# Performance work log

Hardware: AMD Instinct MI355X
Metric: run time of the kernel (lower is better)

Reference implementation:

```python
import jax, jax.numpy as jnp
import numpy as np

B, N, S, C, H = 16, 64, 4096, 768, 8
HD = C // H
SCALE = HD ** -0.5
ASSIGN_EPS = 1.0


def hard_softmax(logits, axis):
    # softmax over `axis`, then straight-through one-hot argmax along `axis`
    y_soft = jax.nn.softmax(logits, axis=axis)
    idx = jnp.argmax(y_soft, axis=axis, keepdims=True)
    n = logits.shape[axis]
    shape = [1] * logits.ndim
    shape[axis] = n
    iota = jnp.arange(n).reshape(shape)
    y_hard = (iota == idx).astype(logits.dtype)
    return y_hard - jax.lax.stop_gradient(y_soft) + y_soft


def setup_inputs() -> dict:
    key = jax.random.key(0)
    ks = jax.random.split(key, 7)
    w = lambda k, shp: (jax.random.normal(k, shp, dtype=jnp.float32) * 0.02)
    return {
        'query': jax.random.normal(ks[0], (B, N, C), dtype=jnp.float32),
        'key_in': jax.random.normal(ks[1], (B, S, C), dtype=jnp.float32),
        'Wq': w(ks[2], (C, C)),
        'Wk': w(ks[3], (C, C)),
        'Wv': w(ks[4], (C, C)),
        'Wo': w(ks[5], (C, C)),
        'bo': jnp.zeros((C,), dtype=jnp.float32),
    }


def reference(query, key_in, Wq, Wk, Wv, Wo, bo):
    # linear projections (torch Linear: x @ W.T), split heads -> b h n d
    q = jnp.einsum('bnc,dc->bnd', query, Wq).reshape(B, N, H, HD).transpose(0, 2, 1, 3)
    k = jnp.einsum('bsc,dc->bsd', key_in, Wk).reshape(B, S, H, HD).transpose(0, 2, 1, 3)
    v = jnp.einsum('bsc,dc->bsd', key_in, Wv).reshape(B, S, H, HD).transpose(0, 2, 1, 3)
    raw_attn = jnp.einsum('bhnd,bhsd->bhns', q, k) * SCALE      # [B,H,N,S]
    attn = hard_softmax(raw_attn, axis=-2)                       # hard assign over groups N
    attn = attn / (attn.sum(axis=-1, keepdims=True) + ASSIGN_EPS)  # renorm over tokens S
    out = jnp.einsum('bhns,bhsd->bhnd', attn, v)                 # [B,H,N,HD]
    out = out.transpose(0, 2, 1, 3).reshape(B, N, C)
    out = jnp.einsum('bnc,dc->bnd', out, Wo) + bo
    return out
```

## Files before the change

kernel.cpp:

```cpp
#include <hip/hip_runtime.h>

#define BB 16
#define NN 64
#define SS 4096
#define CC 768
#define HH 8
#define HD 96

typedef __attribute__((ext_vector_type(8))) short bf16x8;
typedef __attribute__((ext_vector_type(4))) float f32x4;
typedef __attribute__((ext_vector_type(8))) unsigned short u16x8;

static __device__ __forceinline__ unsigned short f2bf(float x) {
  unsigned u = __float_as_uint(x);
  unsigned r = (u + 0x7fffu + ((u >> 16) & 1u)) >> 16;
  return (unsigned short)r;
}
static __device__ __forceinline__ float bf2f(unsigned short h) {
  return __uint_as_float(((unsigned)h) << 16);
}
static __device__ __forceinline__ void split2t(float f0, float f1,
                                               unsigned* hw, unsigned* lw) {
  unsigned u0 = __float_as_uint(f0), u1 = __float_as_uint(f1);
  *hw = (u0 >> 16) | (u1 & 0xffff0000u);
  float l0 = f0 - __uint_as_float(u0 & 0xffff0000u);
  float l1 = f1 - __uint_as_float(u1 & 0xffff0000u);
  unsigned v0 = __float_as_uint(l0), v1 = __float_as_uint(l1);
  *lw = (v0 >> 16) | (v1 & 0xffff0000u);
}

__global__ __launch_bounds__(256) void k_transpose(
    const float* __restrict__ src, float* __restrict__ dst) {
  __shared__ float tile[32][33];
  const int bx = blockIdx.x % 24, by = blockIdx.x / 24;
  const int tx = threadIdx.x & 31, ty = threadIdx.x >> 5;
#pragma unroll
  for (int k = 0; k < 4; ++k)
    tile[ty + k * 8][tx] = src[(size_t)(by * 32 + ty + k * 8) * CC + bx * 32 + tx];
  __syncthreads();
#pragma unroll
  for (int k = 0; k < 4; ++k)
    dst[(size_t)(bx * 32 + ty + k * 8) * CC + by * 32 + tx] = tile[tx][ty + k * 8];
}

__global__ __launch_bounds__(256) void k_q(
    const float* __restrict__ query, const float* __restrict__ WqT,
    double* __restrict__ q64g) {
  __shared__ double qin[2][CC];
  const int tid = threadIdx.x;
  const int rp = blockIdx.x / 3, cs = blockIdx.x % 3;
  const int r0 = rp * 2;

#pragma unroll
  for (int u = 0; u < 6; ++u) {
    int idx = tid + u * 256;
    int r = idx / CC, c = idx - r * CC;
    qin[r][c] = (double)query[(size_t)(r0 + r) * CC + c];
  }
  __syncthreads();

  const int j = cs * 256 + tid;
  double a0 = 0.0, a1 = 0.0;
  const float* wt = WqT + j;
  for (int e = 0; e < CC; ++e) {
    const double w = (double)wt[(size_t)e * CC];
    a0 += qin[0][e] * w;
    a1 += qin[1][e] * w;
  }
  q64g[(size_t)(r0 + 0) * CC + j] = a0;
  q64g[(size_t)(r0 + 1) * CC + j] = a1;
}

__global__ __launch_bounds__(256) void k_fold(
    const double* __restrict__ q64g, const float* __restrict__ Wk,
    double* __restrict__ qk64, unsigned short* __restrict__ qhp,
    unsigned short* __restrict__ qlp) {
  __shared__ double q64l[2][CC];
  const int tid = threadIdx.x;
  const int rp = blockIdx.x / 3, cs3 = blockIdx.x % 3;
  const int r0 = rp * 2;

#pragma unroll
  for (int u = 0; u < 6; ++u) {
    int idx = tid + u * 256;
    int r = idx / CC, c = idx - r * CC;
    q64l[r][c] = q64g[(size_t)(r0 + r) * CC + c];
  }
  __syncthreads();

  const int c = cs3 * 256 + tid;
  const double SC = 0.10206207261596575;
  const int csp = c >> 5, lkc = (c >> 3) & 3, jp = c & 7;

  for (int h = 0; h < HH; ++h) {
    double b0 = 0.0, b1 = 0.0;
    const float* wk = Wk + (size_t)(h * HD) * CC + c;
    const double* qh0 = &q64l[0][h * HD];
    const double* qh1 = &q64l[1][h * HD];
#pragma unroll 4
    for (int dd = 0; dd < HD; ++dd) {
      const double w = (double)wk[(size_t)dd * CC];
      b0 += qh0[dd] * w;
      b1 += qh1[dd] * w;
    }
    b0 *= SC; b1 *= SC;
    double av[2] = {b0, b1};
#pragma unroll
    for (int r = 0; r < 2; ++r) {
      const int row = r0 + r, b_ = row >> 6, n = row & 63;
      const int col512 = h * 64 + n;
      size_t o = ((size_t)(b_ * HH + h) * NN + n) * CC + c;
      qk64[o] = av[r];
      float f = (float)av[r];
      unsigned short hh16 = f2bf(f);
      size_t po = (((size_t)(b_ * 24 + csp) * 32 + (col512 >> 4)) * 64 +
                   (lkc * 16 + (col512 & 15))) * 8 + jp;
      qhp[po] = hh16;
      qlp[po] = f2bf(f - bf2f(hh16));
    }
  }
}

#define DELTA 1e-3f

__global__ __launch_bounds__(512) void k_filter_mfma(
    const float* __restrict__ key,
    const unsigned short* __restrict__ qhp, const unsigned short* __restrict__ qlp,
    unsigned char* __restrict__ assign_t, int* __restrict__ susp,
    int* __restrict__ scnt) {
  __shared__ unsigned short khi[2][64][72];
  __shared__ unsigned short klo[2][64][72];
  const int tid = threadIdx.x;
  const int lane = tid & 63;
  const int wn = tid >> 6;
  const int bid0 = blockIdx.x;
  const int swz = (bid0 & 7) * 128 + (bid0 >> 3);
  const int b = swz >> 6;
  const int s0 = (swz & 63) * 64;
  const int l16 = lane & 15;
  const int lk = lane >> 4;

  f32x4 acc[4][4];
#pragma unroll
  for (int m = 0; m < 4; ++m)
#pragma unroll
    for (int n = 0; n < 4; ++n) acc[m][n] = (f32x4){0.f, 0.f, 0.f, 0.f};

  const float* kbase = key + ((size_t)b * SS + s0) * CC;
  const int srow = tid >> 3, sc8 = tid & 7;

#define BBASE(cs) ((((size_t)(b * 24 + (cs)) * 32 + wn * 4) * 64 + lane) * 8)

  bf16x8 bhA[4], blA[4], bhB[4], blB[4];
  {
    float4 st0 = *(const float4*)(kbase + (size_t)srow * CC + sc8 * 8);
    float4 st1 = *(const float4*)(kbase + (size_t)srow * CC + sc8 * 8 + 4);
    union { u16x8 v; unsigned w[4]; } h8, l8;
    split2t(st0.x, st0.y, &h8.w[0], &l8.w[0]);
    split2t(st0.z, st0.w, &h8.w[1], &l8.w[1]);
    split2t(st1.x, st1.y, &h8.w[2], &l8.w[2]);
    split2t(st1.z, st1.w, &h8.w[3], &l8.w[3]);
    *(u16x8*)&khi[0][srow][sc8 * 8] = h8.v;
    *(u16x8*)&klo[0][srow][sc8 * 8] = l8.v;
    const size_t bb = BBASE(0);
#pragma unroll
    for (int n = 0; n < 4; ++n) {
      bhA[n] = *(const bf16x8*)(qhp + bb + (size_t)n * 512);
      blA[n] = *(const bf16x8*)(qlp + bb + (size_t)n * 512);
    }
  }
  __syncthreads();

  for (int t = 0; t < 12; ++t) {
    const int cur = t & 1;
    float4 st0, st1;
    if (t < 11) {
      const int cb = (t + 1) * 64;
      st0 = *(const float4*)(kbase + (size_t)srow * CC + cb + sc8 * 8);
      st1 = *(const float4*)(kbase + (size_t)srow * CC + cb + sc8 * 8 + 4);
    }
    {
      const int cs = t * 2;
      const size_t bbn = BBASE(cs + 1);
#pragma unroll
      for (int n = 0; n < 4; ++n) {
        bhB[n] = *(const bf16x8*)(qhp + bbn + (size_t)n * 512);
        blB[n] = *(const bf16x8*)(qlp + bbn + (size_t)n * 512);
      }
      bf16x8 ah[4], al_[4];
#pragma unroll
      for (int m = 0; m < 4; ++m) {
        ah[m]  = *(const bf16x8*)&khi[cur][m * 16 + l16][lk * 8];
        al_[m] = *(const bf16x8*)&klo[cur][m * 16 + l16][lk * 8];
      }
#pragma unroll
      for (int m = 0; m < 4; ++m)
#pragma unroll
        for (int n = 0; n < 4; ++n)
          acc[m][n] = __builtin_amdgcn_mfma_f32_16x16x32_bf16(ah[m], bhA[n], acc[m][n], 0, 0, 0);
#pragma unroll
      for (int m = 0; m < 4; ++m)
#pragma unroll
        for (int n = 0; n < 4; ++n)
          acc[m][n] = __builtin_amdgcn_mfma_f32_16x16x32_bf16(ah[m], blA[n], acc[m][n], 0, 0, 0);
#pragma unroll
      for (int m = 0; m < 4; ++m)
#pragma unroll
        for (int n = 0; n < 4; ++n)
          acc[m][n] = __builtin_amdgcn_mfma_f32_16x16x32_bf16(al_[m], bhA[n], acc[m][n], 0, 0, 0);
    }
    {
      if (t < 11) {
        const size_t bbn = BBASE(t * 2 + 2);
#pragma unroll
        for (int n = 0; n < 4; ++n) {
          bhA[n] = *(const bf16x8*)(qhp + bbn + (size_t)n * 512);
          blA[n] = *(const bf16x8*)(qlp + bbn + (size_t)n * 512);
        }
      }
      bf16x8 ah[4], al_[4];
#pragma unroll
      for (int m = 0; m < 4; ++m) {
        ah[m]  = *(const bf16x8*)&khi[cur][m * 16 + l16][32 + lk * 8];
        al_[m] = *(const bf16x8*)&klo[cur][m * 16 + l16][32 + lk * 8];
      }
#pragma unroll
      for (int m = 0; m < 4; ++m)
#pragma unroll
        for (int n = 0; n < 4; ++n)
          acc[m][n] = __builtin_amdgcn_mfma_f32_16x16x32_bf16(ah[m], bhB[n], acc[m][n], 0, 0, 0);
#pragma unroll
      for (int m = 0; m < 4; ++m)
#pragma unroll
        for (int n = 0; n < 4; ++n)
          acc[m][n] = __builtin_amdgcn_mfma_f32_16x16x32_bf16(ah[m], blB[n], acc[m][n], 0, 0, 0);
#pragma unroll
      for (int m = 0; m < 4; ++m)
#pragma unroll
        for (int n = 0; n < 4; ++n)
          acc[m][n] = __builtin_amdgcn_mfma_f32_16x16x32_bf16(al_[m], bhB[n], acc[m][n], 0, 0, 0);
    }

    if (t < 11) {
      union { u16x8 v; unsigned w[4]; } h8, l8;
      split2t(st0.x, st0.y, &h8.w[0], &l8.w[0]);
      split2t(st0.z, st0.w, &h8.w[1], &l8.w[1]);
      split2t(st1.x, st1.y, &h8.w[2], &l8.w[2]);
      split2t(st1.z, st1.w, &h8.w[3], &l8.w[3]);
      *(u16x8*)&khi[cur ^ 1][srow][sc8 * 8] = h8.v;
      *(u16x8*)&klo[cur ^ 1][srow][sc8 * 8] = l8.v;
    }
    __syncthreads();
  }
#undef BBASE

#pragma unroll
  for (int m = 0; m < 4; ++m) {
    const int tokbase = s0 + m * 16 + lk * 4;
#pragma unroll
    for (int r = 0; r < 4; ++r) {
      const int tok = tokbase + r;
      float m1 = -3.402823466e38f, m2 = -3.402823466e38f;
      int i1 = 0;
#pragma unroll
      for (int n = 0; n < 4; ++n) {
        float v = acc[m][n][r];
        int g = n * 16 + l16;
        if (v > m1) { m2 = m1; m1 = v; i1 = g; }
        else if (v > m2) m2 = v;
      }
#pragma unroll
      for (int off = 1; off <= 8; off <<= 1) {
        float om1 = __shfl_xor(m1, off);
        float om2 = __shfl_xor(m2, off);
        int oi1 = __shfl_xor(i1, off);
        if (om1 > m1 || (om1 == m1 && oi1 < i1)) {
          m2 = fmaxf(m1, fmaxf(m2, om2));
          m1 = om1; i1 = oi1;
        } else {
          m2 = fmaxf(om1, fmaxf(m2, om2));
        }
      }
      if (l16 == 0) {
        const int bh2 = b * 8 + wn;
        assign_t[((size_t)b * SS + tok) * 8 + wn] = (unsigned char)i1;
        if (m1 - m2 < DELTA) {
          int w = atomicAdd(&scnt[bh2], 1);
          susp[(size_t)bh2 * SS + w] = tok;
        }
      }
    }
  }
}

__global__ __launch_bounds__(256) void k_rescore(
    const float* __restrict__ key, const double* __restrict__ qk64,
    const int* __restrict__ susp, const int* __restrict__ scnt,
    unsigned char* __restrict__ assign_t) {
  __shared__ float krow[16][CC];
  __shared__ double l64[16][64];
  const int bh = blockIdx.x;
  const int cnt = scnt[bh];
  if (cnt == 0) return;
  const int b = bh >> 3, h = bh & 7;
  const int tid = threadIdx.x;
  const int n = tid >> 2, q = tid & 3;
  const double* qrow = qk64 + ((size_t)bh * NN + n) * CC + q * 192;

  for (int i0 = 0; i0 < cnt; i0 += 16) {
    const int nb = (cnt - i0 < 16) ? (cnt - i0) : 16;
    for (int r = 0; r < nb; ++r) {
      const int s = susp[(size_t)bh * SS + i0 + r];
      for (int u = tid; u < CC; u += 256)
        krow[r][u] = key[((size_t)b * SS + s) * CC + u];
    }
    __syncthreads();

    double acc[16];
#pragma unroll
    for (int r = 0; r < 16; ++r) acc[r] = 0.0;
    for (int c4 = 0; c4 < 48; ++c4) {
      const double w0 = qrow[c4 * 4 + 0];
      const double w1 = qrow[c4 * 4 + 1];
      const double w2 = qrow[c4 * 4 + 2];
      const double w3 = qrow[c4 * 4 + 3];
#pragma unroll
      for (int r = 0; r < 16; ++r) {
        float4 k4 = *(const float4*)&krow[r][q * 192 + c4 * 4];
        acc[r] += w0 * (double)k4.x;
        acc[r] += w1 * (double)k4.y;
        acc[r] += w2 * (double)k4.z;
        acc[r] += w3 * (double)k4.w;
      }
    }
#pragma unroll
    for (int r = 0; r < 16; ++r) {
      acc[r] += __shfl_xor(acc[r], 1);
      acc[r] += __shfl_xor(acc[r], 2);
    }
    if (q == 0) {
#pragma unroll
      for (int r = 0; r < 16; ++r) l64[r][n] = acc[r];
    }
    __syncthreads();
    if (tid < nb) {
      double best = l64[tid][0];
      int bi = 0;
      for (int n2 = 1; n2 < 64; ++n2)
        if (l64[tid][n2] > best) { best = l64[tid][n2]; bi = n2; }
      const int s = susp[(size_t)bh * SS + i0 + tid];
      assign_t[((size_t)b * SS + s) * 8 + h] = (unsigned char)bi;
    }
    __syncthreads();
  }
}

__global__ __launch_bounds__(256) void k_counts(
    const unsigned char* __restrict__ assign_t, int* __restrict__ counts) {
  __shared__ int hist[64];
  const int bh = blockIdx.x;
  const int b = bh >> 3, h = bh & 7;
  const int tid = threadIdx.x;
  if (tid < 64) hist[tid] = 0;
  __syncthreads();
  for (int s = tid; s < SS; s += 256)
    atomicAdd(&hist[assign_t[((size_t)b * SS + s) * 8 + h]], 1);
  __syncthreads();
  if (tid < 64) counts[bh * 64 + tid] = hist[tid];
}

__global__ __launch_bounds__(256) void k_convert(
    const float* __restrict__ keyhalf, unsigned short* __restrict__ kb16) {
  const int n8 = 8 * SS * CC / 8;
  int i = blockIdx.x * 256 + threadIdx.x;
  const int stride = gridDim.x * 256;
  for (; i < n8; i += stride) {
    float4 a = ((const float4*)keyhalf)[i * 2];
    float4 b = ((const float4*)keyhalf)[i * 2 + 1];
    u16x8 r;
    r[0] = f2bf(a.x); r[1] = f2bf(a.y); r[2] = f2bf(a.z); r[3] = f2bf(a.w);
    r[4] = f2bf(b.x); r[5] = f2bf(b.y); r[6] = f2bf(b.z); r[7] = f2bf(b.w);
    *(u16x8*)(kb16 + (size_t)i * 8) = r;
  }
}

__global__ __launch_bounds__(64) void k_rank(
    const unsigned char* __restrict__ assign_t, const int* __restrict__ counts,
    int* __restrict__ offsets, int* __restrict__ perm) {
  __shared__ int base[64];
  const int bh = blockIdx.x;
  const int b = bh >> 3, h = bh & 7;
  const int lane = threadIdx.x;

  int cn = counts[bh * 64 + lane];
  int off = cn;
#pragma unroll
  for (int d = 1; d < 64; d <<= 1) {
    int t = __shfl_up(off, d);
    if (lane >= d) off += t;
  }
  off -= cn;
  offsets[bh * 64 + lane] = off;
  base[lane] = off;

  for (int c = 0; c < SS / 64; ++c) {
    const int s = c * 64 + lane;
    const int g = (int)assign_t[((size_t)b * SS + s) * 8 + h];
    unsigned long long m = ~0ull;
#pragma unroll
    for (int k = 0; k < 6; ++k) {
      unsigned long long bk = __ballot((g >> k) & 1);
      m &= ((g >> k) & 1) ? bk : ~bk;
    }
    const int leader = __ffsll((unsigned long long)m) - 1;
    const int rankin = __popcll(m & ((1ull << lane) - 1ull));
    int baseo = 0;
    if (lane == leader) {
      baseo = base[g];
      base[g] = baseo + __popcll(m);
    }
    baseo = __shfl(baseo, leader);
    perm[(size_t)bh * SS + baseo + rankin] = s;
  }
}

__global__ __launch_bounds__(64) void k_gatherp(
    const unsigned short* __restrict__ kb16, const int* __restrict__ perm,
    const int* __restrict__ offsets, const int* __restrict__ counts,
    float* __restrict__ gsum, int b0) {
  const int bid = blockIdx.x;
  const int bl = bid >> 9;
  const int gbid = b0 * 512 + bid;
  const int bh = gbid >> 6;
  const int lane = threadIdx.x;

  const int off = offsets[gbid];
  const int cnt = counts[gbid];
  const int* pl = perm + (size_t)bh * SS + off;
  const unsigned short* kb = kb16 + (size_t)bl * SS * CC;

  float4 a0 = {0.f, 0.f, 0.f, 0.f}, b0v = a0, c0 = a0;
  int j = 0;
  for (; j + 3 < cnt; j += 4) {
    const int s0 = pl[j], s1 = pl[j + 1], s2 = pl[j + 2], s3 = pl[j + 3];
    const ushort4* k0 = (const ushort4*)(kb + (size_t)s0 * CC);
    const ushort4* k1 = (const ushort4*)(kb + (size_t)s1 * CC);
    const ushort4* k2 = (const ushort4*)(kb + (size_t)s2 * CC);
    const ushort4* k3 = (const ushort4*)(kb + (size_t)s3 * CC);
    ushort4 x0 = k0[lane], x1 = k0[lane + 64], x2 = k0[lane + 128];
    ushort4 y0 = k1[lane], y1 = k1[lane + 64], y2 = k1[lane + 128];
    ushort4 z0 = k2[lane], z1 = k2[lane + 64], z2 = k2[lane + 128];
    ushort4 w0 = k3[lane], w1 = k3[lane + 64], w2 = k3[lane + 128];
    a0.x += bf2f(x0.x); a0.y += bf2f(x0.y); a0.z += bf2f(x0.z); a0.w += bf2f(x0.w);
    b0v.x += bf2f(x1.x); b0v.y += bf2f(x1.y); b0v.z += bf2f(x1.z); b0v.w += bf2f(x1.w);
    c0.x += bf2f(x2.x); c0.y += bf2f(x2.y); c0.z += bf2f(x2.z); c0.w += bf2f(x2.w);
    a0.x += bf2f(y0.x); a0.y += bf2f(y0.y); a0.z += bf2f(y0.z); a0.w += bf2f(y0.w);
    b0v.x += bf2f(y1.x); b0v.y += bf2f(y1.y); b0v.z += bf2f(y1.z); b0v.w += bf2f(y1.w);
    c0.x += bf2f(y2.x); c0.y += bf2f(y2.y); c0.z += bf2f(y2.z); c0.w += bf2f(y2.w);
    a0.x += bf2f(z0.x); a0.y += bf2f(z0.y); a0.z += bf2f(z0.z); a0.w += bf2f(z0.w);
    b0v.x += bf2f(z1.x); b0v.y += bf2f(z1.y); b0v.z += bf2f(z1.z); b0v.w += bf2f(z1.w);
    c0.x += bf2f(z2.x); c0.y += bf2f(z2.y); c0.z += bf2f(z2.z); c0.w += bf2f(z2.w);
    a0.x += bf2f(w0.x); a0.y += bf2f(w0.y); a0.z += bf2f(w0.z); a0.w += bf2f(w0.w);
    b0v.x += bf2f(w1.x); b0v.y += bf2f(w1.y); b0v.z += bf2f(w1.z); b0v.w += bf2f(w1.w);
    c0.x += bf2f(w2.x); c0.y += bf2f(w2.y); c0.z += bf2f(w2.z); c0.w += bf2f(w2.w);
  }
  for (; j < cnt; ++j) {
    const int s0 = pl[j];
    const ushort4* k0 = (const ushort4*)(kb + (size_t)s0 * CC);
    ushort4 x0 = k0[lane], x1 = k0[lane + 64], x2 = k0[lane + 128];
    a0.x += bf2f(x0.x); a0.y += bf2f(x0.y); a0.z += bf2f(x0.z); a0.w += bf2f(x0.w);
    b0v.x += bf2f(x1.x); b0v.y += bf2f(x1.y); b0v.z += bf2f(x1.z); b0v.w += bf2f(x1.w);
    c0.x += bf2f(x2.x); c0.y += bf2f(x2.y); c0.z += bf2f(x2.z); c0.w += bf2f(x2.w);
  }
  float4* go = (float4*)(gsum + (size_t)gbid * CC);
  go[lane] = a0; go[lane + 64] = b0v; go[lane + 128] = c0;
}

__global__ __launch_bounds__(256) void k_out(
    const float* __restrict__ gsum, const int* __restrict__ counts,
    const float* __restrict__ WvT, const float* __restrict__ WoT,
    const float* __restrict__ bo, float* __restrict__ out) {
  __shared__ float gs[2][HH][CC];
  __shared__ float vr[2][CC];
  const int tid = threadIdx.x;
  const int r0 = blockIdx.x * 2;

  for (int r = 0; r < 2; ++r) {
    int row = r0 + r, b = row >> 6, n = row & 63;
    for (int h = 0; h < HH; ++h) {
      const float sc = 1.f / (float)(counts[(b * HH + h) * NN + n] + 1);
      const float* src = gsum + ((size_t)(b * HH + h) * NN + n) * CC;
      for (int m = 0; m < 3; ++m)
        gs[r][h][tid + m * 256] = src[tid + m * 256] * sc;
    }
  }
  __syncthreads();

  const int h0 = tid / HD, h1 = (tid + 256) / HD, h2 = (tid + 512) / HD;
  {
    float a00 = 0.f, a01 = 0.f, a02 = 0.f;
    float a10 = 0.f, a11 = 0.f, a12 = 0.f;
    const float* wt = WvT + tid;
    for (int e4 = 0; e4 < CC / 4; ++e4) {
      const int e = e4 * 4;
      float4 g00 = *(const float4*)&gs[0][h0][e];
      float4 g01 = *(const float4*)&gs[0][h1][e];
      float4 g02 = *(const float4*)&gs[0][h2][e];
      float4 g10 = *(const float4*)&gs[1][h0][e];
      float4 g11 = *(const float4*)&gs[1][h1][e];
      float4 g12 = *(const float4*)&gs[1][h2][e];
      const float* w0p = wt + (size_t)e * CC;
      const float* w1p = wt + (size_t)(e + 1) * CC;
      const float* w2p = wt + (size_t)(e + 2) * CC;
      const float* w3p = wt + (size_t)(e + 3) * CC;
      float wa = w0p[0], wb = w0p[256], wc = w0p[512];
      a00 = fmaf(g00.x, wa, a00); a01 = fmaf(g01.x, wb, a01); a02 = fmaf(g02.x, wc, a02);
      a10 = fmaf(g10.x, wa, a10); a11 = fmaf(g11.x, wb, a11); a12 = fmaf(g12.x, wc, a12);
      wa = w1p[0]; wb = w1p[256]; wc = w1p[512];
      a00 = fmaf(g00.y, wa, a00); a01 = fmaf(g01.y, wb, a01); a02 = fmaf(g02.y, wc, a02);
      a10 = fmaf(g10.y, wa, a10); a11 = fmaf(g11.y, wb, a11); a12 = fmaf(g12.y, wc, a12);
      wa = w2p[0]; wb = w2p[256]; wc = w2p[512];
      a00 = fmaf(g00.z, wa, a00); a01 = fmaf(g01.z, wb, a01); a02 = fmaf(g02.z, wc, a02);
      a10 = fmaf(g10.z, wa, a10); a11 = fmaf(g11.z, wb, a11); a12 = fmaf(g12.z, wc, a12);
      wa = w3p[0]; wb = w3p[256]; wc = w3p[512];
      a00 = fmaf(g00.w, wa, a00); a01 = fmaf(g01.w, wb, a01); a02 = fmaf(g02.w, wc, a02);
      a10 = fmaf(g10.w, wa, a10); a11 = fmaf(g11.w, wb, a11); a12 = fmaf(g12.w, wc, a12);
    }
    vr[0][tid] = a00; vr[0][tid + 256] = a01; vr[0][tid + 512] = a02;
    vr[1][tid] = a10; vr[1][tid + 256] = a11; vr[1][tid + 512] = a12;
  }
  __syncthreads();

  {
    float a00 = bo[tid], a01 = bo[tid + 256], a02 = bo[tid + 512];
    float a10 = a00, a11 = a01, a12 = a02;
    const float* wt = WoT + tid;
    for (int e4 = 0; e4 < CC / 4; ++e4) {
      const int e = e4 * 4;
      float4 v0 = *(const float4*)&vr[0][e];
      float4 v1 = *(const float4*)&vr[1][e];
      const float* w0p = wt + (size_t)e * CC;
      const float* w1p = wt + (size_t)(e + 1) * CC;
      const float* w2p = wt + (size_t)(e + 2) * CC;
      const float* w3p = wt + (size_t)(e + 3) * CC;
      float wa = w0p[0], wb = w0p[256], wc = w0p[512];
      a00 = fmaf(v0.x, wa, a00); a01 = fmaf(v0.x, wb, a01); a02 = fmaf(v0.x, wc, a02);
      a10 = fmaf(v1.x, wa, a10); a11 = fmaf(v1.x, wb, a11); a12 = fmaf(v1.x, wc, a12);
      wa = w1p[0]; wb = w1p[256]; wc = w1p[512];
      a00 = fmaf(v0.y, wa, a00); a01 = fmaf(v0.y, wb, a01); a02 = fmaf(v0.y, wc, a02);
      a10 = fmaf(v1.y, wa, a10); a11 = fmaf(v1.y, wb, a11); a12 = fmaf(v1.y, wc, a12);
      wa = w2p[0]; wb = w2p[256]; wc = w2p[512];
      a00 = fmaf(v0.z, wa, a00); a01 = fmaf(v0.z, wb, a01); a02 = fmaf(v0.z, wc, a02);
      a10 = fmaf(v1.z, wa, a10); a11 = fmaf(v1.z, wb, a11); a12 = fmaf(v1.z, wc, a12);
      wa = w3p[0]; wb = w3p[256]; wc = w3p[512];
      a00 = fmaf(v0.w, wa, a00); a01 = fmaf(v0.w, wb, a01); a02 = fmaf(v0.w, wc, a02);
      a10 = fmaf(v1.w, wa, a10); a11 = fmaf(v1.w, wb, a11); a12 = fmaf(v1.w, wc, a12);
    }
    out[(size_t)(r0 + 0) * CC + tid] = a00;
    out[(size_t)(r0 + 0) * CC + tid + 256] = a01;
    out[(size_t)(r0 + 0) * CC + tid + 512] = a02;
    out[(size_t)(r0 + 1) * CC + tid] = a10;
    out[(size_t)(r0 + 1) * CC + tid + 256] = a11;
    out[(size_t)(r0 + 1) * CC + tid + 512] = a12;
  }
}

extern "C" void kernel_launch(void* const* d_in, const int* in_sizes, int n_in,
                              void* d_out, int out_size, void* d_ws, size_t ws_size,
                              hipStream_t stream) {
  const float* query = (const float*)d_in[0];
  const float* key   = (const float*)d_in[1];
  const float* Wq    = (const float*)d_in[2];
  const float* Wk    = (const float*)d_in[3];
  const float* Wv    = (const float*)d_in[4];
  const float* Wo    = (const float*)d_in[5];
  const float* bo    = (const float*)d_in[6];
  float* out = (float*)d_out;

  char* ws = (char*)d_ws;
  double* qk64           = (double*)(ws);
  unsigned short* kb16   = (unsigned short*)(ws);
  unsigned short* qhp    = (unsigned short*)(ws + 50331648);
  unsigned short* qlp    = (unsigned short*)(ws + 62914560);
  float* gsum            = (float*)(ws + 50331648);
  unsigned char* assign_t= (unsigned char*)(ws + 75497472);
  int* susp              = (int*)(ws + 76021760);
  int* scnt              = (int*)(ws + 78118912);
  int* counts            = (int*)(ws + 78119424);
  int* offsets           = (int*)(ws + 78152192);
  int* perm              = (int*)(ws + 78184960);
  float* WqT             = (float*)(ws + 80282112);
  float* WvT             = (float*)(ws + 82641408);
  float* WoT             = (float*)(ws + 85000704);
  double* q64g           = (double*)(ws + 87360000);

  hipMemsetAsync(scnt, 0, 512, stream);
  k_transpose<<<576, 256, 0, stream>>>(Wq, WqT);
  k_transpose<<<576, 256, 0, stream>>>(Wv, WvT);
  k_transpose<<<576, 256, 0, stream>>>(Wo, WoT);
  k_q<<<1536, 256, 0, stream>>>(query, WqT, q64g);
  k_fold<<<1536, 256, 0, stream>>>(q64g, Wk, qk64, qhp, qlp);
  k_filter_mfma<<<1024, 512, 0, stream>>>(key, qhp, qlp, assign_t, susp, scnt);
  k_rescore<<<128, 256, 0, stream>>>(key, qk64, susp, scnt, assign_t);
  k_counts<<<128, 256, 0, stream>>>(assign_t, counts);
  k_rank<<<128, 64, 0, stream>>>(assign_t, counts, offsets, perm);
  k_convert<<<1024, 256, 0, stream>>>(key, kb16);
  k_gatherp<<<4096, 64, 0, stream>>>(kb16, perm, offsets, counts, gsum, 0);
  k_convert<<<1024, 256, 0, stream>>>(key + (size_t)8 * SS * CC, kb16);
  k_gatherp<<<4096, 64, 0, stream>>>(kb16, perm, offsets, counts, gsum, 8);
  k_out<<<512, 256, 0, stream>>>(gsum, counts, WvT, WoT, bo, out);
}
```

Measured before the change: 805.0 us.

## Split filter MFMA blocks into two 4-head halves with 256 threads

The filter kernel now launches twice as many 256-thread blocks, each covering 4 of the 8 heads for a 64-token tile, instead of one 512-thread block covering all heads. Each thread stages 16 key floats per step instead of 8, and the prefetch loads are issued inside the staging macro after the MFMAs rather than before them. This aims for better occupancy and scheduling flexibility, but every key tile is now read and split into hi/lo bf16 twice, and the global-load latency is no longer hidden behind the MFMA work.

```diff
diff --git a/kernel.cpp b/kernel.cpp
--- a/kernel.cpp
+++ b/kernel.cpp
@@ -123,7 +123,7 @@
 
 #define DELTA 1e-3f
 
-__global__ __launch_bounds__(512) void k_filter_mfma(
+__global__ __launch_bounds__(256) void k_filter_mfma(
     const float* __restrict__ key,
     const unsigned short* __restrict__ qhp, const unsigned short* __restrict__ qlp,
     unsigned char* __restrict__ assign_t, int* __restrict__ susp,
@@ -133,10 +133,12 @@
   const int tid = threadIdx.x;
   const int lane = tid & 63;
   const int wn = tid >> 6;
-  const int bid0 = blockIdx.x;
-  const int swz = (bid0 & 7) * 128 + (bid0 >> 3);
+  const int bid = blockIdx.x;
+  const int pid0 = bid >> 1, hh4 = bid & 1;
+  const int swz = (pid0 & 7) * 128 + (pid0 >> 3);
   const int b = swz >> 6;
   const int s0 = (swz & 63) * 64;
+  const int head = hh4 * 4 + wn;
   const int l16 = lane & 15;
   const int lk = lane >> 4;
 
@@ -147,21 +149,34 @@
     for (int n = 0; n < 4; ++n) acc[m][n] = (f32x4){0.f, 0.f, 0.f, 0.f};
 
   const float* kbase = key + ((size_t)b * SS + s0) * CC;
-  const int srow = tid >> 3, sc8 = tid & 7;
-
-#define BBASE(cs) ((((size_t)(b * 24 + (cs)) * 32 + wn * 4) * 64 + lane) * 8)
+  const int srow = tid >> 2, c16 = (tid & 3) * 16;
+
+#define BBASE(cs) ((((size_t)(b * 24 + (cs)) * 32 + head * 4) * 64 + lane) * 8)
+#define STAGE(buf, cb)                                                         \
+  {                                                                            \
+    const float* sp = kbase + (size_t)srow * CC + (cb) + c16;                  \
+    float4 x0 = *(const float4*)(sp);                                          \
+    float4 x1 = *(const float4*)(sp + 4);                                      \
+    float4 x2 = *(const float4*)(sp + 8);                                      \
+    float4 x3 = *(const float4*)(sp + 12);                                     \
+    union { u16x8 v; unsigned w[4]; } ha, la, hb, lb;                          \
+    split2t(x0.x, x0.y, &ha.w[0], &la.w[0]);                                   \
+    split2t(x0.z, x0.w, &ha.w[1], &la.w[1]);                                   \
+    split2t(x1.x, x1.y, &ha.w[2], &la.w[2]);                                   \
+    split2t(x1.z, x1.w, &ha.w[3], &la.w[3]);                                   \
+    split2t(x2.x, x2.y, &hb.w[0], &lb.w[0]);                                   \
+    split2t(x2.z, x2.w, &hb.w[1], &lb.w[1]);                                   \
+    split2t(x3.x, x3.y, &hb.w[2], &lb.w[2]);                                   \
+    split2t(x3.z, x3.w, &hb.w[3], &lb.w[3]);                                   \
+    *(u16x8*)&khi[buf][srow][c16] = ha.v;                                      \
+    *(u16x8*)&khi[buf][srow][c16 + 8] = hb.v;                                  \
+    *(u16x8*)&klo[buf][srow][c16] = la.v;                                      \
+    *(u16x8*)&klo[buf][srow][c16 + 8] = lb.v;                                  \
+  }
 
   bf16x8 bhA[4], blA[4], bhB[4], blB[4];
   {
-    float4 st0 = *(const float4*)(kbase + (size_t)srow * CC + sc8 * 8);
-    float4 st1 = *(const float4*)(kbase + (size_t)srow * CC + sc8 * 8 + 4);
-    union { u16x8 v; unsigned w[4]; } h8, l8;
-    split2t(st0.x, st0.y, &h8.w[0], &l8.w[0]);
-    split2t(st0.z, st0.w, &h8.w[1], &l8.w[1]);
-    split2t(st1.x, st1.y, &h8.w[2], &l8.w[2]);
-    split2t(st1.z, st1.w, &h8.w[3], &l8.w[3]);
-    *(u16x8*)&khi[0][srow][sc8 * 8] = h8.v;
-    *(u16x8*)&klo[0][srow][sc8 * 8] = l8.v;
+    STAGE(0, 0);
     const size_t bb = BBASE(0);
 #pragma unroll
     for (int n = 0; n < 4; ++n) {
@@ -173,12 +188,6 @@
 
   for (int t = 0; t < 12; ++t) {
     const int cur = t & 1;
-    float4 st0, st1;
-    if (t < 11) {
-      const int cb = (t + 1) * 64;
-      st0 = *(const float4*)(kbase + (size_t)srow * CC + cb + sc8 * 8);
-      st1 = *(const float4*)(kbase + (size_t)srow * CC + cb + sc8 * 8 + 4);
-    }
     {
       const int cs = t * 2;
       const size_t bbn = BBASE(cs + 1);
@@ -242,16 +251,11 @@
     }
 
     if (t < 11) {
-      union { u16x8 v; unsigned w[4]; } h8, l8;
-      split2t(st0.x, st0.y, &h8.w[0], &l8.w[0]);
-      split2t(st0.z, st0.w, &h8.w[1], &l8.w[1]);
-      split2t(st1.x, st1.y, &h8.w[2], &l8.w[2]);
-      split2t(st1.z, st1.w, &h8.w[3], &l8.w[3]);
-      *(u16x8*)&khi[cur ^ 1][srow][sc8 * 8] = h8.v;
-      *(u16x8*)&klo[cur ^ 1][srow][sc8 * 8] = l8.v;
+      STAGE(cur ^ 1, (t + 1) * 64);
     }
     __syncthreads();
   }
+#undef STAGE
 #undef BBASE
 
 #pragma unroll
@@ -282,8 +286,8 @@
         }
       }
       if (l16 == 0) {
-        const int bh2 = b * 8 + wn;
-        assign_t[((size_t)b * SS + tok) * 8 + wn] = (unsigned char)i1;
+        const int bh2 = b * 8 + head;
+        assign_t[((size_t)b * SS + tok) * 8 + head] = (unsigned char)i1;
         if (m1 - m2 < DELTA) {
           int w = atomicAdd(&scnt[bh2], 1);
           susp[(size_t)bh2 * SS + w] = tok;
@@ -600,7 +604,7 @@
   k_transpose<<<576, 256, 0, stream>>>(Wo, WoT);
   k_q<<<1536, 256, 0, stream>>>(query, WqT, q64g);
   k_fold<<<1536, 256, 0, stream>>>(q64g, Wk, qk64, qhp, qlp);
-  k_filter_mfma<<<1024, 512, 0, stream>>>(key, qhp, qlp, assign_t, susp, scnt);
+  k_filter_mfma<<<2048, 256, 0, stream>>>(key, qhp, qlp, assign_t, susp, scnt);
   k_rescore<<<128, 256, 0, stream>>>(key, qk64, susp, scnt, assign_t);
   k_counts<<<128, 256, 0, stream>>>(assign_t, counts);
   k_rank<<<128, 64, 0, stream>>>(assign_t, counts, offsets, perm);
```

After: 806.3 us. No clear change (+0.2%).
